# Kernel tuning notes

Hardware: AMD Instinct MI355X
Metric: run time of the kernel (lower is better)

Reference implementation:

```python
import jax, jax.numpy as jnp
import numpy as np
import math

B, L, N, DIM, H = 2, 8, 1024, 512, 8
DH = DIM // H

def setup_inputs() -> dict:
    key = jax.random.key(0)
    ks = jax.random.split(key, 9)
    s = 1.0 / math.sqrt(DIM)
    return {
        "x": jax.random.normal(ks[0], (B, L, N, DIM), dtype=jnp.float32),
        "Wq": jax.random.normal(ks[1], (DIM, DIM), dtype=jnp.float32) * s,
        "bq": jnp.zeros((DIM,), dtype=jnp.float32),
        "Wk": jax.random.normal(ks[2], (DIM, DIM), dtype=jnp.float32) * s,
        "bk": jnp.zeros((DIM,), dtype=jnp.float32),
        "Wv": jax.random.normal(ks[3], (DIM, DIM), dtype=jnp.float32) * s,
        "bv": jnp.zeros((DIM,), dtype=jnp.float32),
        "Wo": jax.random.normal(ks[4], (DIM, DIM), dtype=jnp.float32) * s,
        "bo": jnp.zeros((DIM,), dtype=jnp.float32),
    }

def _split_heads(t):
    # 'b l n (h d) -> b l h n d'
    b, l, n, _ = t.shape
    return t.reshape(b, l, n, H, DH).transpose(0, 1, 3, 2, 4)

def reference(x, Wq, bq, Wk, bk, Wv, bv, Wo, bo):
    q = _split_heads(x @ Wq.T + bq)
    # FAITHFUL BUG: source maps (q, v, k) -> (q_mat, k_mat, v_mat),
    # so the "keys" come from the v projection and "values" from the k projection.
    k_mat = _split_heads(x @ Wv.T + bv)
    v_mat = _split_heads(x @ Wk.T + bk)
    # scale is sqrt(Dh * num_heads) = sqrt(dim), as in the source
    scores = jnp.einsum('blhnd,blhmd->blhnm', q, k_mat) / math.sqrt(DIM)
    weights = jax.nn.softmax(scores, axis=-1)
    inter = jnp.einsum('blhnm,blhmd->blhnd', weights, v_mat)
    # 'b l h n d -> b l n (h d)'
    inter = inter.transpose(0, 1, 3, 2, 4).reshape(x.shape[0], x.shape[1], x.shape[2], DIM)
    return inter @ Wo.T + bo
```

## Files before the change

### kernel.cpp

```cpp
#include <hip/hip_runtime.h>
#include <stdint.h>

#define DIMC 512
#define NSEQ 1024
#define BLT  16
#define NHEAD 8
#define DHD  64
#define MTOT (BLT*NSEQ)

typedef float f32x4 __attribute__((ext_vector_type(4)));
typedef float f32x16 __attribute__((ext_vector_type(16)));
typedef short s16x8 __attribute__((ext_vector_type(8)));
typedef short s16x4 __attribute__((ext_vector_type(4)));

__device__ __forceinline__ unsigned short f2bf(float f) {
    unsigned int u = __float_as_uint(f);
    u += 0x7fffu + ((u >> 16) & 1u);
    return (unsigned short)(u >> 16);
}
__device__ __forceinline__ float bf2f(unsigned short h) {
    return __uint_as_float(((unsigned int)h) << 16);
}

#define QSCALE (0.04419417382415922f * 1.4426950408889634f)

__device__ __forceinline__ void gll16(const void* g, void* l) {
    __builtin_amdgcn_global_load_lds(
        (const __attribute__((address_space(1))) void*)g,
        (__attribute__((address_space(3))) void*)l, 16, 0, 0);
}

__device__ __forceinline__ unsigned int cvtpk(float lo, float hi) {
    unsigned int r;
    asm("v_cvt_pk_bf16_f32 %0, %1, %2" : "=v"(r) : "v"(lo), "v"(hi));
    return r;
}

__device__ __forceinline__ void pl32swap(unsigned int &a, unsigned int &b) {
    asm volatile("v_permlane32_swap_b32 %0, %1" : "+v"(a), "+v"(b));
}

__device__ __forceinline__ bool detect_bf16(const unsigned short* x) {
    int t = threadIdx.x & 63;
    unsigned short v = x[2 * t];
    int e = (v >> 7) & 0xFF;
    unsigned long long ball = __ballot(e < 100 || e > 137);
    return __popcll(ball) < 16;
}

struct ConvArgs {
    const void* src[9];
    unsigned short* dst[9];
};

__global__ __launch_bounds__(256) void conv_kernel(ConvArgs a,
                                                   const unsigned short* __restrict__ xdet) {
    const bool isbf = detect_bf16(xdet);
    int b = blockIdx.x;
    int seg, idx;
    if (b < 4096)      { seg = 0; idx = (b * 256 + threadIdx.x) * 8; }
    else if (b < 4608) { int t = b - 4096; seg = 1 + (t >> 7);
                         idx = (((t & 127) * 256) + threadIdx.x) * 8; }
    else               { int i = threadIdx.x * 8; seg = 5 + (i >> 9); idx = i & 511; }
    const void* s = a.src[seg];
    unsigned short* d = a.dst[seg];
    if (isbf) {
        *(uint4*)(d + idx) = *(const uint4*)((const unsigned short*)s + idx);
    } else {
        float4 t0 = *(const float4*)((const float*)s + idx);
        float4 t1 = *(const float4*)((const float*)s + idx + 4);
        ushort4 v0{f2bf(t0.x), f2bf(t0.y), f2bf(t0.z), f2bf(t0.w)};
        ushort4 v1{f2bf(t1.x), f2bf(t1.y), f2bf(t1.z), f2bf(t1.w)};
        *(ushort4*)(d + idx)     = v0;
        *(ushort4*)(d + idx + 4) = v1;
    }
}

__device__ __forceinline__ void gemm_core_async(
    const unsigned short* __restrict__ Ap, const unsigned short* __restrict__ Wp,
    int mBase, int nBase, unsigned short* Al, unsigned short* Bl, f32x4 acc[4][4])
{
    const int wave = threadIdx.x >> 6;
    const int lane = threadIdx.x & 63;
    const int lr = lane & 15, lg = lane >> 4;
    const int wm = wave >> 1, wn = wave & 1;
    const int srow = lane >> 3;
    const int scol = (lane & 7) * 8;

    #pragma unroll
    for (int a = 0; a < 4; ++a)
        #pragma unroll
        for (int b = 0; b < 4; ++b) acc[a][b] = (f32x4){0.f, 0.f, 0.f, 0.f};

    for (int k0 = 0; k0 < DIMC; k0 += 64) {
        #pragma unroll
        for (int i = 0; i < 4; ++i) {
            int rbase = (wave * 4 + i) * 8;
            gll16(Ap + (long)(mBase + rbase + srow) * DIMC + k0 + scol, Al + rbase * 64);
            gll16(Wp + (long)(nBase + rbase + srow) * DIMC + k0 + scol, Bl + rbase * 64);
        }
        __syncthreads();

        #pragma unroll
        for (int kk = 0; kk < 64; kk += 32) {
            s16x8 af[4], bf_[4];
            #pragma unroll
            for (int a = 0; a < 4; ++a)
                af[a] = *(const s16x8*)&Al[(wm * 64 + a * 16 + lr) * 64 + kk + lg * 8];
            #pragma unroll
            for (int b = 0; b < 4; ++b)
                bf_[b] = *(const s16x8*)&Bl[(wn * 64 + b * 16 + lr) * 64 + kk + lg * 8];
            #pragma unroll
            for (int a = 0; a < 4; ++a)
                #pragma unroll
                for (int b = 0; b < 4; ++b)
                    acc[a][b] = __builtin_amdgcn_mfma_f32_16x16x32_bf16(af[a], bf_[b], acc[a][b], 0, 0, 0);
        }
        __syncthreads();
    }
}

__global__ __launch_bounds__(256) void proj_kernel(
    const unsigned short* __restrict__ xb,
    const unsigned short* __restrict__ Wqb, const unsigned short* __restrict__ Wkb,
    const unsigned short* __restrict__ Wvb,
    const unsigned short* __restrict__ bqb, const unsigned short* __restrict__ bkb,
    const unsigned short* __restrict__ bvb,
    unsigned short* __restrict__ Q, unsigned short* __restrict__ K,
    unsigned short* __restrict__ Vt)
{
    const int bid = blockIdx.x;
    const int xcd = bid & 7;
    const int s = bid >> 3;
    const int z = s >> 6;
    const int r = s & 63;
    const int mt = ((r >> 2) << 3) + xcd;
    const int nt = r & 3;

    const unsigned short* Wp = (z == 0) ? Wqb : ((z == 1) ? Wvb : Wkb);
    const unsigned short* bp = (z == 0) ? bqb : ((z == 1) ? bvb : bkb);
    unsigned short* outp = (z == 0) ? Q : ((z == 1) ? K : Vt);
    const float oscale = (z == 0) ? QSCALE : 1.0f;

    const int mBase = mt * 128;
    const int nBase = nt * 128;
    const int lane = threadIdx.x & 63;
    const int lr = lane & 15, lg = lane >> 4;
    const int wm = (threadIdx.x >> 6) >> 1, wn = (threadIdx.x >> 6) & 1;

    __shared__ unsigned short Al[128 * 64];
    __shared__ unsigned short Bl[128 * 64];
    f32x4 acc[4][4];
    gemm_core_async(xb, Wp, mBase, nBase, Al, Bl, acc);

    #pragma unroll
    for (int b = 0; b < 4; ++b) {
        int j = nBase + wn * 64 + b * 16 + lr;
        float bb = bf2f(bp[j]);
        int h = j >> 6, d = j & 63;
        #pragma unroll
        for (int a = 0; a < 4; ++a) {
            int m0 = mBase + wm * 64 + a * 16 + lg * 4;
            int bl = m0 >> 10, n0 = m0 & 1023;
            if (z == 2) {
                ushort4 pk;
                unsigned short* p = (unsigned short*)&pk;
                #pragma unroll
                for (int r2 = 0; r2 < 4; ++r2) p[r2] = f2bf(acc[a][b][r2] + bb);
                *(ushort4*)&outp[(((bl << 3) + h) << 16) + (d << 10) + n0] = pk;
            } else {
                #pragma unroll
                for (int r2 = 0; r2 < 4; ++r2) {
                    float v = (acc[a][b][r2] + bb) * oscale;
                    outp[(((bl << 3) + h) << 16) + ((n0 + r2) << 6) + d] = f2bf(v);
                }
            }
        }
    }
}

__global__ __launch_bounds__(256) void out_gemm_kernel(
    const unsigned short* __restrict__ inter, const unsigned short* __restrict__ Wob,
    const unsigned short* __restrict__ bob, void* __restrict__ outp,
    const unsigned short* __restrict__ xdet)
{
    const bool isbf = detect_bf16(xdet);
    const int bid = blockIdx.x;
    const int xcd = bid & 7;
    const int s = bid >> 3;
    const int mt = ((s >> 2) << 3) + xcd;
    const int nt = s & 3;

    const int mBase = mt * 128;
    const int nBase = nt * 128;
    const int lane = threadIdx.x & 63;
    const int lr = lane & 15, lg = lane >> 4;
    const int wm = (threadIdx.x >> 6) >> 1, wn = (threadIdx.x >> 6) & 1;

    __shared__ unsigned short Al[128 * 64];
    __shared__ unsigned short Bl[128 * 64];
    f32x4 acc[4][4];
    gemm_core_async(inter, Wob, mBase, nBase, Al, Bl, acc);

    #pragma unroll
    for (int b = 0; b < 4; ++b) {
        int j = nBase + wn * 64 + b * 16 + lr;
        float bb = bf2f(bob[j]);
        #pragma unroll
        for (int a = 0; a < 4; ++a) {
            #pragma unroll
            for (int r = 0; r < 4; ++r) {
                long m = mBase + wm * 64 + a * 16 + lg * 4 + r;
                float v = acc[a][b][r] + bb;
                if (isbf) ((unsigned short*)outp)[m * DIMC + j] = f2bf(v);
                else      ((float*)outp)[m * DIMC + j] = v;
            }
        }
    }
}

#define SWZ(row, col) ((row) * 64 + ((col) ^ (((row) & 7) * 8)))

__global__ __launch_bounds__(256, 3) void attn_kernel(
    const unsigned short* __restrict__ Q, const unsigned short* __restrict__ K,
    const unsigned short* __restrict__ Vt, unsigned short* __restrict__ inter)
{
    const int b = blockIdx.x;
    const int bh = b & 127;
    const int qt = b >> 7;
    const int tid = threadIdx.x;
    const int wave = tid >> 6;
    const int lane = tid & 63;
    const int l31 = lane & 31;
    const int hi = lane >> 5;

    const unsigned short* Qb = Q + (long)bh * (NSEQ * DHD);
    const int qbase = qt * 128 + wave * 32;

    s16x8 qf[4];
    #pragma unroll
    for (int k16 = 0; k16 < 4; ++k16)
        qf[k16] = *(const s16x8*)&Qb[(qbase + l31) * DHD + k16 * 16 + hi * 8];

    __shared__ unsigned short Kl[2][64 * 64];
    __shared__ unsigned short Vl[2][64 * 64];

    const int srow = tid >> 3;
    const int scol = ((tid & 7) * 8) ^ ((srow & 7) * 8);
    const unsigned short* kp = K  + (long)bh * (NSEQ * DHD) + srow * DHD  + scol;
    const unsigned short* vp = Vt + (long)bh * (NSEQ * DHD) + srow * NSEQ + scol;

    auto stage = [&](int buf, long ko, long vo) {
        unsigned short* Kb_ = &Kl[buf][0];
        unsigned short* Vb_ = &Vl[buf][0];
        gll16(kp + ko,         Kb_ + wave * 512);
        gll16(kp + ko + 2048,  Kb_ + wave * 512 + 2048);
        gll16(vp + vo,         Vb_ + wave * 512);
        gll16(vp + vo + 32768, Vb_ + wave * 512 + 2048);
    };

    f32x16 o[2];
    f32x16 lacc;
    f32x16 zero16;
    #pragma unroll
    for (int r = 0; r < 16; ++r) { o[0][r] = 0.f; o[1][r] = 0.f; lacc[r] = 0.f; zero16[r] = 0.f; }
    const s16x8 ones8 = {(short)0x3F80, (short)0x3F80, (short)0x3F80, (short)0x3F80,
                         (short)0x3F80, (short)0x3F80, (short)0x3F80, (short)0x3F80};

    stage(0, 0, 0);
    __syncthreads();

    #pragma unroll 2
    for (int kt = 0; kt < 16; ++kt) {
        const int cur = kt & 1;
        if (kt < 15)
            stage(cur ^ 1, (long)(kt + 1) * (64 * DHD), (long)(kt + 1) * 64);

        const unsigned short* Kc = &Kl[cur][0];
        const unsigned short* Vc = &Vl[cur][0];

        #pragma unroll
        for (int kc = 0; kc < 2; ++kc) {
            s16x8 af[4];
            #pragma unroll
            for (int k16 = 0; k16 < 4; ++k16)
                af[k16] = *(const s16x8*)&Kc[SWZ(kc * 32 + l31, k16 * 16 + hi * 8)];
            f32x16 s;
            __builtin_amdgcn_s_setprio(1);
            s = __builtin_amdgcn_mfma_f32_32x32x16_bf16(af[0], qf[0], zero16, 0, 0, 0);
            s = __builtin_amdgcn_mfma_f32_32x32x16_bf16(af[1], qf[1], s, 0, 0, 0);
            s = __builtin_amdgcn_mfma_f32_32x32x16_bf16(af[2], qf[2], s, 0, 0, 0);
            s = __builtin_amdgcn_mfma_f32_32x32x16_bf16(af[3], qf[3], s, 0, 0, 0);
            __builtin_amdgcn_s_setprio(0);

            float p[16];
            #pragma unroll
            for (int r = 0; r < 16; ++r) p[r] = __builtin_exp2f(s[r]);
            unsigned int w[4][2];
            #pragma unroll
            for (int b4 = 0; b4 < 4; ++b4) {
                w[b4][0] = cvtpk(p[4 * b4 + 0], p[4 * b4 + 1]);
                w[b4][1] = cvtpk(p[4 * b4 + 2], p[4 * b4 + 3]);
            }
            s16x8 frag[2];
            #pragma unroll
            for (int t16 = 0; t16 < 2; ++t16) {
                unsigned int a0 = w[2 * t16][0], b0 = w[2 * t16 + 1][0];
                unsigned int a1 = w[2 * t16][1], b1 = w[2 * t16 + 1][1];
                pl32swap(a0, b0);
                pl32swap(a1, b1);
                union { unsigned int u[4]; s16x8 v; } f;
                f.u[0] = a0; f.u[1] = a1; f.u[2] = b0; f.u[3] = b1;
                frag[t16] = f.v;
            }

            s16x8 va[2][2];
            #pragma unroll
            for (int dt = 0; dt < 2; ++dt)
                #pragma unroll
                for (int t16 = 0; t16 < 2; ++t16)
                    va[dt][t16] = *(const s16x8*)&Vc[SWZ(dt * 32 + l31, kc * 32 + t16 * 16 + hi * 8)];
            __builtin_amdgcn_s_setprio(1);
            lacc = __builtin_amdgcn_mfma_f32_32x32x16_bf16(ones8, frag[0], lacc, 0, 0, 0);
            lacc = __builtin_amdgcn_mfma_f32_32x32x16_bf16(ones8, frag[1], lacc, 0, 0, 0);
            #pragma unroll
            for (int dt = 0; dt < 2; ++dt)
                #pragma unroll
                for (int t16 = 0; t16 < 2; ++t16)
                    o[dt] = __builtin_amdgcn_mfma_f32_32x32x16_bf16(va[dt][t16], frag[t16], o[dt], 0, 0, 0);
            __builtin_amdgcn_s_setprio(0);
        }

        if (kt < 15) __syncthreads();
    }

    const int bl = bh >> 3, h = bh & 7;
    const int q = qbase + l31;
    float inv = 1.f / lacc[0];
    #pragma unroll
    for (int dt = 0; dt < 2; ++dt) {
        #pragma unroll
        for (int b4 = 0; b4 < 4; ++b4) {
            unsigned int w0 = cvtpk(o[dt][4 * b4 + 0] * inv, o[dt][4 * b4 + 1] * inv);
            unsigned int w1 = cvtpk(o[dt][4 * b4 + 2] * inv, o[dt][4 * b4 + 3] * inv);
            union { unsigned int u[2]; ushort4 v; } pk;
            pk.u[0] = w0; pk.u[1] = w1;
            *(ushort4*)&inter[((long)(bl * NSEQ + q)) * DIMC + h * 64 + dt * 32 + 8 * b4 + 4 * hi] = pk.v;
        }
    }
}

extern "C" void kernel_launch(void* const* d_in, const int* in_sizes, int n_in,
                              void* d_out, int out_size, void* d_ws, size_t ws_size,
                              hipStream_t stream) {
    const void* x  = d_in[0];
    const void* Wq = d_in[1]; const void* bq = d_in[2];
    const void* Wk = d_in[3]; const void* bk = d_in[4];
    const void* Wv = d_in[5]; const void* bv = d_in[6];
    const void* Wo = d_in[7]; const void* bo = d_in[8];

    char* ws = (char*)d_ws;
    unsigned short* xb  = (unsigned short*)ws;
    unsigned short* Q   = xb + (long)MTOT * DIMC;
    unsigned short* K   = Q  + (long)MTOT * DIMC;
    unsigned short* Vt  = K  + (long)MTOT * DIMC;
    unsigned short* Wqb = Vt + (long)MTOT * DIMC;
    unsigned short* Wkb = Wqb + DIMC * DIMC;
    unsigned short* Wvb = Wkb + DIMC * DIMC;
    unsigned short* Wob = Wvb + DIMC * DIMC;
    unsigned short* bqb = Wob + DIMC * DIMC;
    unsigned short* bkb = bqb + DIMC;
    unsigned short* bvb = bkb + DIMC;
    unsigned short* bob = bvb + DIMC;

    ConvArgs ca;
    ca.src[0] = x;  ca.src[1] = Wq; ca.src[2] = Wk; ca.src[3] = Wv; ca.src[4] = Wo;
    ca.src[5] = bq; ca.src[6] = bk; ca.src[7] = bv; ca.src[8] = bo;
    ca.dst[0] = xb;  ca.dst[1] = Wqb; ca.dst[2] = Wkb; ca.dst[3] = Wvb; ca.dst[4] = Wob;
    ca.dst[5] = bqb; ca.dst[6] = bkb; ca.dst[7] = bvb; ca.dst[8] = bob;
    conv_kernel<<<4609, 256, 0, stream>>>(ca, (const unsigned short*)x);

    proj_kernel<<<1536, 256, 0, stream>>>(xb, Wqb, Wkb, Wvb, bqb, bkb, bvb, Q, K, Vt);

    attn_kernel<<<8 * 128, 256, 0, stream>>>(Q, K, Vt, xb );

    out_gemm_kernel<<<512, 256, 0, stream>>>(xb , Wob, bob, d_out,
                                             (const unsigned short*)x);
}
```

Measured before the change: 214.4 us.

## Fuse Q/K/V projections into one block sharing the x tile

The projection kernel now computes all three Q, V and K outputs in one 512-thread block instead of launching a separate block per projection. Each x tile is loaded into shared memory once and reused against three weight tiles, which cuts x global reads threefold and shrinks the grid from 1536 to 512 blocks. The cost is more shared memory (four 16KB tiles), 24 accumulators per thread and fewer blocks, which may lower occupancy and latency hiding.

Measured after the change: 243.8 us. 13.7% more time.

```diff
diff --git a/kernel.cpp b/kernel.cpp
--- a/kernel.cpp
+++ b/kernel.cpp
@@ -76,51 +76,7 @@
     }
 }
 
-__device__ __forceinline__ void gemm_core_async(
-    const unsigned short* __restrict__ Ap, const unsigned short* __restrict__ Wp,
-    int mBase, int nBase, unsigned short* Al, unsigned short* Bl, f32x4 acc[4][4])
-{
-    const int wave = threadIdx.x >> 6;
-    const int lane = threadIdx.x & 63;
-    const int lr = lane & 15, lg = lane >> 4;
-    const int wm = wave >> 1, wn = wave & 1;
-    const int srow = lane >> 3;
-    const int scol = (lane & 7) * 8;
-
-    #pragma unroll
-    for (int a = 0; a < 4; ++a)
-        #pragma unroll
-        for (int b = 0; b < 4; ++b) acc[a][b] = (f32x4){0.f, 0.f, 0.f, 0.f};
-
-    for (int k0 = 0; k0 < DIMC; k0 += 64) {
-        #pragma unroll
-        for (int i = 0; i < 4; ++i) {
-            int rbase = (wave * 4 + i) * 8;
-            gll16(Ap + (long)(mBase + rbase + srow) * DIMC + k0 + scol, Al + rbase * 64);
-            gll16(Wp + (long)(nBase + rbase + srow) * DIMC + k0 + scol, Bl + rbase * 64);
-        }
-        __syncthreads();
-
-        #pragma unroll
-        for (int kk = 0; kk < 64; kk += 32) {
-            s16x8 af[4], bf_[4];
-            #pragma unroll
-            for (int a = 0; a < 4; ++a)
-                af[a] = *(const s16x8*)&Al[(wm * 64 + a * 16 + lr) * 64 + kk + lg * 8];
-            #pragma unroll
-            for (int b = 0; b < 4; ++b)
-                bf_[b] = *(const s16x8*)&Bl[(wn * 64 + b * 16 + lr) * 64 + kk + lg * 8];
-            #pragma unroll
-            for (int a = 0; a < 4; ++a)
-                #pragma unroll
-                for (int b = 0; b < 4; ++b)
-                    acc[a][b] = __builtin_amdgcn_mfma_f32_16x16x32_bf16(af[a], bf_[b], acc[a][b], 0, 0, 0);
-        }
-        __syncthreads();
-    }
-}
-
-__global__ __launch_bounds__(256) void proj_kernel(
+__global__ __launch_bounds__(512, 4) void proj_kernel(
     const unsigned short* __restrict__ xb,
     const unsigned short* __restrict__ Wqb, const unsigned short* __restrict__ Wkb,
     const unsigned short* __restrict__ Wvb,
@@ -132,50 +88,138 @@
     const int bid = blockIdx.x;
     const int xcd = bid & 7;
     const int s = bid >> 3;
-    const int z = s >> 6;
-    const int r = s & 63;
-    const int mt = ((r >> 2) << 3) + xcd;
-    const int nt = r & 3;
-
-    const unsigned short* Wp = (z == 0) ? Wqb : ((z == 1) ? Wvb : Wkb);
-    const unsigned short* bp = (z == 0) ? bqb : ((z == 1) ? bvb : bkb);
-    unsigned short* outp = (z == 0) ? Q : ((z == 1) ? K : Vt);
-    const float oscale = (z == 0) ? QSCALE : 1.0f;
-
+    const int mt = ((s >> 2) << 3) + xcd;
+    const int nt = s & 3;
     const int mBase = mt * 128;
     const int nBase = nt * 128;
+
+    const int tid = threadIdx.x;
+    const int wave = tid >> 6;
+    const int lane = tid & 63;
+    const int lr = lane & 15, lg = lane >> 4;
+    const int wm = wave >> 2, wn = wave & 3;
+
+    __shared__ unsigned short Al[128 * 64];
+    __shared__ unsigned short Bl[3][128 * 64];
+
+    f32x4 acc[3][4][2];
+    #pragma unroll
+    for (int z = 0; z < 3; ++z)
+        #pragma unroll
+        for (int a = 0; a < 4; ++a)
+            #pragma unroll
+            for (int b = 0; b < 2; ++b) acc[z][a][b] = (f32x4){0.f, 0.f, 0.f, 0.f};
+
+    const unsigned short* Ws[3] = {Wqb, Wvb, Wkb};
+
+    const int srow = lane >> 3;
+    const int scol = (lane & 7) * 8;
+
+    for (int k0 = 0; k0 < DIMC; k0 += 64) {
+        #pragma unroll
+        for (int r = 0; r < 2; ++r) {
+            int row = r * 64 + wave * 8;
+            gll16(xb + (long)(mBase + row + srow) * DIMC + k0 + scol, Al + row * 64);
+            #pragma unroll
+            for (int z = 0; z < 3; ++z)
+                gll16(Ws[z] + (long)(nBase + row + srow) * DIMC + k0 + scol,
+                      Bl[z] + row * 64);
+        }
+        __syncthreads();
+
+        #pragma unroll
+        for (int kk = 0; kk < 64; kk += 32) {
+            s16x8 af[4];
+            #pragma unroll
+            for (int a = 0; a < 4; ++a)
+                af[a] = *(const s16x8*)&Al[(wm * 64 + a * 16 + lr) * 64 + kk + lg * 8];
+            #pragma unroll
+            for (int z = 0; z < 3; ++z) {
+                s16x8 bf0 = *(const s16x8*)&Bl[z][(wn * 32 + lr) * 64 + kk + lg * 8];
+                s16x8 bf1 = *(const s16x8*)&Bl[z][(wn * 32 + 16 + lr) * 64 + kk + lg * 8];
+                #pragma unroll
+                for (int a = 0; a < 4; ++a) {
+                    acc[z][a][0] = __builtin_amdgcn_mfma_f32_16x16x32_bf16(af[a], bf0, acc[z][a][0], 0, 0, 0);
+                    acc[z][a][1] = __builtin_amdgcn_mfma_f32_16x16x32_bf16(af[a], bf1, acc[z][a][1], 0, 0, 0);
+                }
+            }
+        }
+        __syncthreads();
+    }
+
+    #pragma unroll
+    for (int z = 0; z < 3; ++z) {
+        const unsigned short* bp = (z == 0) ? bqb : ((z == 1) ? bvb : bkb);
+        unsigned short* outp = (z == 0) ? Q : ((z == 1) ? K : Vt);
+        const float oscale = (z == 0) ? QSCALE : 1.0f;
+        #pragma unroll
+        for (int b = 0; b < 2; ++b) {
+            int j = nBase + wn * 32 + b * 16 + lr;
+            float bb = bf2f(bp[j]);
+            int h = j >> 6, d = j & 63;
+            #pragma unroll
+            for (int a = 0; a < 4; ++a) {
+                int m0 = mBase + wm * 64 + a * 16 + lg * 4;
+                int bl = m0 >> 10, n0 = m0 & 1023;
+                if (z == 2) {
+                    ushort4 pk;
+                    unsigned short* p = (unsigned short*)&pk;
+                    #pragma unroll
+                    for (int r2 = 0; r2 < 4; ++r2) p[r2] = f2bf(acc[z][a][b][r2] + bb);
+                    *(ushort4*)&outp[(((bl << 3) + h) << 16) + (d << 10) + n0] = pk;
+                } else {
+                    #pragma unroll
+                    for (int r2 = 0; r2 < 4; ++r2) {
+                        float v = (acc[z][a][b][r2] + bb) * oscale;
+                        outp[(((bl << 3) + h) << 16) + ((n0 + r2) << 6) + d] = f2bf(v);
+                    }
+                }
+            }
+        }
+    }
+}
+
+__device__ __forceinline__ void gemm_core_async(
+    const unsigned short* __restrict__ Ap, const unsigned short* __restrict__ Wp,
+    int mBase, int nBase, unsigned short* Al, unsigned short* Bl, f32x4 acc[4][4])
+{
+    const int wave = threadIdx.x >> 6;
     const int lane = threadIdx.x & 63;
     const int lr = lane & 15, lg = lane >> 4;
-    const int wm = (threadIdx.x >> 6) >> 1, wn = (threadIdx.x >> 6) & 1;
-
-    __shared__ unsigned short Al[128 * 64];
-    __shared__ unsigned short Bl[128 * 64];
-    f32x4 acc[4][4];
-    gemm_core_async(xb, Wp, mBase, nBase, Al, Bl, acc);
-
-    #pragma unroll
-    for (int b = 0; b < 4; ++b) {
-        int j = nBase + wn * 64 + b * 16 + lr;
-        float bb = bf2f(bp[j]);
-        int h = j >> 6, d = j & 63;
-        #pragma unroll
-        for (int a = 0; a < 4; ++a) {
-            int m0 = mBase + wm * 64 + a * 16 + lg * 4;
-            int bl = m0 >> 10, n0 = m0 & 1023;
-            if (z == 2) {
-                ushort4 pk;
-                unsigned short* p = (unsigned short*)&pk;
+    const int wm = wave >> 1, wn = wave & 1;
+    const int srow = lane >> 3;
+    const int scol = (lane & 7) * 8;
+
+    #pragma unroll
+    for (int a = 0; a < 4; ++a)
+        #pragma unroll
+        for (int b = 0; b < 4; ++b) acc[a][b] = (f32x4){0.f, 0.f, 0.f, 0.f};
+
+    for (int k0 = 0; k0 < DIMC; k0 += 64) {
+        #pragma unroll
+        for (int i = 0; i < 4; ++i) {
+            int rbase = (wave * 4 + i) * 8;
+            gll16(Ap + (long)(mBase + rbase + srow) * DIMC + k0 + scol, Al + rbase * 64);
+            gll16(Wp + (long)(nBase + rbase + srow) * DIMC + k0 + scol, Bl + rbase * 64);
+        }
+        __syncthreads();
+
+        #pragma unroll
+        for (int kk = 0; kk < 64; kk += 32) {
+            s16x8 af[4], bf_[4];
+            #pragma unroll
+            for (int a = 0; a < 4; ++a)
+                af[a] = *(const s16x8*)&Al[(wm * 64 + a * 16 + lr) * 64 + kk + lg * 8];
+            #pragma unroll
+            for (int b = 0; b < 4; ++b)
+                bf_[b] = *(const s16x8*)&Bl[(wn * 64 + b * 16 + lr) * 64 + kk + lg * 8];
+            #pragma unroll
+            for (int a = 0; a < 4; ++a)
                 #pragma unroll
-                for (int r2 = 0; r2 < 4; ++r2) p[r2] = f2bf(acc[a][b][r2] + bb);
-                *(ushort4*)&outp[(((bl << 3) + h) << 16) + (d << 10) + n0] = pk;
-            } else {
-                #pragma unroll
-                for (int r2 = 0; r2 < 4; ++r2) {
-                    float v = (acc[a][b][r2] + bb) * oscale;
-                    outp[(((bl << 3) + h) << 16) + ((n0 + r2) << 6) + d] = f2bf(v);
-                }
-            }
-        }
+                for (int b = 0; b < 4; ++b)
+                    acc[a][b] = __builtin_amdgcn_mfma_f32_16x16x32_bf16(af[a], bf_[b], acc[a][b], 0, 0, 0);
+        }
+        __syncthreads();
     }
 }
 
@@ -380,7 +424,7 @@
     ca.dst[5] = bqb; ca.dst[6] = bkb; ca.dst[7] = bvb; ca.dst[8] = bob;
     conv_kernel<<<4609, 256, 0, stream>>>(ca, (const unsigned short*)x);
 
-    proj_kernel<<<1536, 256, 0, stream>>>(xb, Wqb, Wkb, Wvb, bqb, bkb, bvb, Q, K, Vt);
+    proj_kernel<<<512, 512, 0, stream>>>(xb, Wqb, Wkb, Wvb, bqb, bkb, bvb, Q, K, Vt);
 
     attn_kernel<<<8 * 128, 256, 0, stream>>>(Q, K, Vt, xb );
 
```
